# Kernel optimization log

Measured on AMD Instinct MI355X. Metric: run time of the kernel, lower is better.

The kernel has to match this reference:

```python
import jax, jax.numpy as jnp
import numpy as np

# Static configuration (mirrors TemporalAugmentation with deterministic choices)
B, T_IN, N, C = 32, 512, 543, 3
SPEED = 1.2                      # fixed draw from speed_range (0.8, 1.2)
NEW_T = int(T_IN / SPEED)        # 426
JITTER_FREQ = max(1, NEW_T // 8) # 53
FRAME_DROP_P = 0.1
JITTER_STD = 0.02
NOISE_STD = 0.01
SPATIAL_STD = 0.005


def linresample(x, out_T):
    """F.interpolate(mode='linear', align_corners=True) along last axis."""
    L = x.shape[-1]
    s = jnp.arange(out_T, dtype=x.dtype) * ((L - 1) / (out_T - 1))
    i0 = jnp.clip(jnp.floor(s).astype(jnp.int32), 0, L - 2)
    frac = s - i0.astype(x.dtype)
    return x[..., i0] * (1 - frac) + x[..., i0 + 1] * frac


def setup_inputs() -> dict:
    key = jax.random.key(0)
    k1, k2, k3, k4, k5 = jax.random.split(key, 5)
    x = jax.random.normal(k1, (B, T_IN, N, C), dtype=jnp.float32)
    mask = jnp.ones((B, T_IN), dtype=bool)
    keep_mask = jax.random.bernoulli(k2, 1.0 - FRAME_DROP_P, (B, NEW_T))
    keep_mask = keep_mask.at[:, 0].set(True).at[:, -1].set(True)
    base_jitter = jax.random.normal(k3, (B, JITTER_FREQ), dtype=jnp.float32)
    noise = jax.random.normal(k4, (B, NEW_T, N, C), dtype=jnp.float32)
    spatial_noise = jax.random.normal(k5, (B, 1, N, C), dtype=jnp.float32)
    return {"x": x, "mask": mask, "keep_mask": keep_mask,
            "base_jitter": base_jitter, "noise": noise,
            "spatial_noise": spatial_noise}


def reference(x, mask, keep_mask, base_jitter, noise, spatial_noise):
    Bb, T, Nn, Cc = x.shape
    # --- speed augment: linear resample time axis T -> NEW_T ---
    xt = jnp.moveaxis(x, 1, -1)                 # (B,N,C,T)
    x = jnp.moveaxis(linresample(xt, NEW_T), -1, 1)  # (B,NEW_T,N,C)
    # nearest resample of validity mask (PyTorch 'nearest': floor(t*in/out))
    nidx = jnp.floor(jnp.arange(NEW_T) * (T / NEW_T)).astype(jnp.int32)
    mask = mask[:, nidx]
    T2 = NEW_T
    # --- frame dropout: replace dropped frames with align_corners linear
    # resample of the kept-frame subsequence (length K) back to T2 ---
    K = keep_mask.sum(axis=1)                   # (B,) kept counts
    ar = jnp.arange(T2)
    # stable order putting kept indices first, in original order
    order = jnp.argsort(jnp.where(keep_mask, ar, T2 + ar), axis=1)  # (B,T2)
    s = ar[None, :].astype(x.dtype) * (K[:, None] - 1).astype(x.dtype) / (T2 - 1)
    r0 = jnp.clip(jnp.floor(s).astype(jnp.int32), 0, (K - 2)[:, None])
    frac = (s - r0.astype(x.dtype))[:, :, None, None]
    bidx = jnp.arange(Bb)[:, None]
    idx0 = jnp.take_along_axis(order, r0, axis=1)
    idx1 = jnp.take_along_axis(order, r0 + 1, axis=1)
    interp = x[bidx, idx0] * (1 - frac) + x[bidx, idx1] * frac
    x = jnp.where(keep_mask[:, :, None, None], x, interp)
    mask = mask & keep_mask
    # --- temporal jitter: scale per-frame velocity by smooth jitter curve ---
    jit = linresample(base_jitter * JITTER_STD, T2)   # (B,T2)
    vel = x[:, 1:] - x[:, :-1]
    x = jnp.concatenate([x[:, :1], x[:, 1:] + vel * jit[:, 1:, None, None]], axis=1)
    # --- coordinate noise + per-landmark spatial noise ---
    x = x + noise * NOISE_STD + spatial_noise * SPATIAL_STD
    return x, mask
```

## Files before the change

### kernel.cpp

```cpp
#include <hip/hip_runtime.h>
#include <stdint.h>

#define B_      32
#define T_IN_   512
#define N_      543
#define C_      3
#define NEW_T_  426
#define JF_     53
#define NC_     (N_*C_)
#define XOUT_   (B_*NEW_T_*NC_)
#define NFR_    (B_*NEW_T_)
#define GPF_    408
#define TOTG_   (NFR_*GPF_)
#define G_      4
#define NBLK_   5432

#define MODE_INT   0
#define MODE_BYTE  1
#define MODE_FLOAT 2

typedef float f4u __attribute__((vector_size(16), aligned(4)));

__device__ __forceinline__ bool read_flag(const void* p, int mode, int idx) {
    if (mode == MODE_BYTE)  return ((const uint8_t*)p)[idx] != 0;
    if (mode == MODE_FLOAT) return ((const float*)p)[idx]   != 0.0f;
    return ((const int*)p)[idx] != 0;
}

__global__ __launch_bounds__(512) void prep_kernel(
    const void* __restrict__ maskp,
    const void* __restrict__ keepp,
    const float* __restrict__ bjit,
    float* __restrict__ out_mask,
    int4*  __restrict__ wsF,
    float4* __restrict__ wsW,
    float* __restrict__ wsJ)
{
    const int b = blockIdx.x;
    const int tid = threadIdx.x;

    __shared__ int flags[6];
    __shared__ int s_mode_mask, s_mode_keep;
    if (tid < 6) flags[tid] = 0;
    __syncthreads();
    if (tid < 64) {
        uint32_t vm = ((const uint32_t*)maskp)[tid];
        uint32_t vk = ((const uint32_t*)keepp)[tid];
        if (vm == 0x3F800000u)      atomicOr(&flags[2], 1);
        else if (vm > 1u)           atomicOr(&flags[1], 1);
        if (vk == 0x3F800000u)      atomicOr(&flags[5], 1);
        else if (vk > 1u)           atomicOr(&flags[4], 1);
    }
    __syncthreads();
    if (tid == 0) {
        s_mode_mask = flags[2] ? MODE_FLOAT : (flags[1] ? MODE_BYTE : MODE_INT);
        s_mode_keep = flags[5] ? MODE_FLOAT : (flags[4] ? MODE_BYTE : MODE_INT);
    }
    __syncthreads();
    const int mmode = s_mode_mask, kmode = s_mode_keep;

    __shared__ int sk[512];
    __shared__ int ps[512];
    __shared__ int kept[NEW_T_];

    int kv = 0;
    if (tid < NEW_T_) kv = read_flag(keepp, kmode, b*NEW_T_ + tid) ? 1 : 0;
    sk[tid] = (tid < NEW_T_) ? kv : 0;
    ps[tid] = sk[tid];
    __syncthreads();
    for (int off = 1; off < 512; off <<= 1) {
        int v = (tid >= off) ? ps[tid - off] : 0;
        __syncthreads();
        ps[tid] += v;
        __syncthreads();
    }
    const int K = ps[NEW_T_ - 1];
    if (tid < NEW_T_ && kv) kept[ps[tid] - 1] = tid;
    __syncthreads();

    if (tid < NEW_T_) {
        const int t = tid;
        const float RATX = (float)(511.0 / 425.0);
        float st = (float)t * RATX;
        int i0 = (int)floorf(st);
        if (i0 < 0) i0 = 0; if (i0 > T_IN_ - 2) i0 = T_IN_ - 2;
        float w = st - (float)i0;

        int4 F; float4 W;
        if (kv) {
            F = make_int4(i0, i0 + 1, i0, i0 + 1);
            W = make_float4(1.0f - w, w, 0.0f, 0.0f);
        } else {
            float s = ((float)t * (float)(K - 1)) / 425.0f;
            int r0 = (int)floorf(s);
            if (r0 < 0) r0 = 0; if (r0 > K - 2) r0 = K - 2;
            float f = s - (float)r0;
            int j0 = kept[r0], j1 = kept[r0 + 1];
            float s0 = (float)j0 * RATX;
            int a0 = (int)floorf(s0);
            if (a0 < 0) a0 = 0; if (a0 > T_IN_ - 2) a0 = T_IN_ - 2;
            float w0 = s0 - (float)a0;
            float s1 = (float)j1 * RATX;
            int a1 = (int)floorf(s1);
            if (a1 < 0) a1 = 0; if (a1 > T_IN_ - 2) a1 = T_IN_ - 2;
            float w1 = s1 - (float)a1;
            F = make_int4(a0, a0 + 1, a1, a1 + 1);
            W = make_float4((1.0f - f) * (1.0f - w0), (1.0f - f) * w0,
                            f * (1.0f - w1),          f * w1);
        }
        const int bt = b * NEW_T_ + t;
        wsF[bt] = F;
        wsW[bt] = W;

        const float RATJ = (float)(52.0 / 425.0);
        float sj = (float)t * RATJ;
        int ji = (int)floorf(sj);
        if (ji < 0) ji = 0; if (ji > JF_ - 2) ji = JF_ - 2;
        float jf = sj - (float)ji;
        float b0 = bjit[b*JF_ + ji]     * 0.02f;
        float b1 = bjit[b*JF_ + ji + 1] * 0.02f;
        float jv = b0 * (1.0f - jf) + b1 * jf;
        if (t == 0) jv = 0.0f;
        wsJ[bt] = jv;

        float mn = (float)t * (float)(512.0 / 426.0);
        int nidx = (int)floorf(mn);
        if (nidx > T_IN_ - 1) nidx = T_IN_ - 1;
        bool mo = read_flag(maskp, mmode, b*T_IN_ + nidx) && (kv != 0);
        out_mask[bt] = mo ? 1.0f : 0.0f;
    }
}

__global__ __launch_bounds__(256) __attribute__((amdgpu_waves_per_eu(2, 8)))
void main_kernel(
    const float* __restrict__ x,
    const float* __restrict__ noise,
    const float* __restrict__ spat,
    const int4*  __restrict__ wsF,
    const float4* __restrict__ wsW,
    const float* __restrict__ wsJ,
    float* __restrict__ out)
{
    const uint32_t S = NBLK_ * 256u;
    const uint32_t g0 = blockIdx.x * 256u + threadIdx.x;

    int4   F[G_], FP[G_];
    float4 W[G_], WP[G_];
    float  JV[G_];
    uint32_t E0[G_], BT[G_], BB[G_];
    bool   VA[G_];

    #pragma unroll
    for (int k = 0; k < G_; k++) {
        uint32_t gid = g0 + (uint32_t)k * S;
        bool v = gid < (uint32_t)TOTG_;
        VA[k] = v;
        uint32_t gc = v ? gid : 0u;
        uint32_t bt = (uint32_t)(((uint64_t)gc * 673720361ull) >> 38);
        uint32_t j  = gc - bt * (uint32_t)GPF_;
        uint32_t e0 = j * 4u; if (e0 > (uint32_t)(NC_ - 4)) e0 = (uint32_t)(NC_ - 4);
        uint32_t b  = (uint32_t)(((uint64_t)bt * 161313326ull) >> 36);
        uint32_t pbt = bt ? bt - 1u : 0u;
        BT[k] = bt; BB[k] = b; E0[k] = e0;
        F[k]  = wsF[bt];  W[k]  = wsW[bt];
        FP[k] = wsF[pbt]; WP[k] = wsW[pbt];
        JV[k] = wsJ[bt];
    }

    f4u T0[G_], T1[G_], T2[G_], T3[G_], Q0[G_], Q1[G_], Q2[G_], Q3[G_], NZ[G_], SP[G_];
    #pragma unroll
    for (int k = 0; k < G_; k++) {
        const float* xb = x + (size_t)BB[k] * (T_IN_ * NC_);
        const uint32_t e0 = E0[k];
        T0[k] = *(const f4u*)(xb + (uint32_t)F[k].x  * NC_ + e0);
        T1[k] = *(const f4u*)(xb + (uint32_t)F[k].y  * NC_ + e0);
        T2[k] = *(const f4u*)(xb + (uint32_t)F[k].z  * NC_ + e0);
        T3[k] = *(const f4u*)(xb + (uint32_t)F[k].w  * NC_ + e0);
        Q0[k] = *(const f4u*)(xb + (uint32_t)FP[k].x * NC_ + e0);
        Q1[k] = *(const f4u*)(xb + (uint32_t)FP[k].y * NC_ + e0);
        Q2[k] = *(const f4u*)(xb + (uint32_t)FP[k].z * NC_ + e0);
        Q3[k] = *(const f4u*)(xb + (uint32_t)FP[k].w * NC_ + e0);
        NZ[k] = *(const f4u*)(noise + (size_t)BT[k] * NC_ + e0);
        SP[k] = *(const f4u*)(spat  + (size_t)BB[k] * NC_ + e0);
    }

    #pragma unroll
    for (int k = 0; k < G_; k++) {
        if (!VA[k]) continue;
        f4u a  = W[k].x  * T0[k] + W[k].y  * T1[k] + W[k].z  * T2[k] + W[k].w  * T3[k];
        f4u ap = WP[k].x * Q0[k] + WP[k].y * Q1[k] + WP[k].z * Q2[k] + WP[k].w * Q3[k];
        f4u r  = a + (a - ap) * JV[k] + NZ[k] * 0.01f + SP[k] * 0.005f;
        *(f4u*)(out + (size_t)BT[k] * NC_ + E0[k]) = r;
    }
}

extern "C" void kernel_launch(void* const* d_in, const int* in_sizes, int n_in,
                              void* d_out, int out_size, void* d_ws, size_t ws_size,
                              hipStream_t stream) {
    const float* x    = (const float*)d_in[0];
    const void*  mask = d_in[1];
    const void*  keep = d_in[2];
    const float* bjit = (const float*)d_in[3];
    const float* noise = (const float*)d_in[4];
    const float* spat  = (const float*)d_in[5];
    float* out = (float*)d_out;

    char* ws = (char*)d_ws;
    int4*   wsF = (int4*)ws;
    float4* wsW = (float4*)(ws + 218112);
    float*  wsJ = (float*)(ws + 436224);

    prep_kernel<<<B_, 512, 0, stream>>>(mask, keep, bjit,
                                        out + XOUT_, wsF, wsW, wsJ);
    main_kernel<<<NBLK_, 256, 0, stream>>>(x, noise, spat, wsF, wsW, wsJ, out);
}
```

Measured before the change: 269.4 us.

## Process consecutive frames per thread, reuse previous interpolation, skip zero-weight gathers

Measured after the change: 255.2 us. 5.3% less time.

```diff
diff --git a/kernel.cpp b/kernel.cpp
--- a/kernel.cpp
+++ b/kernel.cpp
@@ -11,9 +11,8 @@
 #define XOUT_   (B_*NEW_T_*NC_)
 #define NFR_    (B_*NEW_T_)
 #define GPF_    408
-#define TOTG_   (NFR_*GPF_)
-#define G_      4
-#define NBLK_   5432
+#define FPB_    6
+#define NTB_    71
 
 #define MODE_INT   0
 #define MODE_BYTE  1
@@ -131,7 +130,7 @@
     }
 }
 
-__global__ __launch_bounds__(256) __attribute__((amdgpu_waves_per_eu(2, 8)))
+__global__ __launch_bounds__(448) __attribute__((amdgpu_waves_per_eu(3, 8)))
 void main_kernel(
     const float* __restrict__ x,
     const float* __restrict__ noise,
@@ -141,56 +140,54 @@
     const float* __restrict__ wsJ,
     float* __restrict__ out)
 {
-    const uint32_t S = NBLK_ * 256u;
-    const uint32_t g0 = blockIdx.x * 256u + threadIdx.x;
-
-    int4   F[G_], FP[G_];
-    float4 W[G_], WP[G_];
-    float  JV[G_];
-    uint32_t E0[G_], BT[G_], BB[G_];
-    bool   VA[G_];
+    const int j = threadIdx.x;
+    if (j >= GPF_) return;
+    const int b  = blockIdx.y;
+    const int t0 = blockIdx.x * FPB_;
+
+    uint32_t e0 = (uint32_t)j * 4u;
+    if (e0 > (uint32_t)(NC_ - 4)) e0 = (uint32_t)(NC_ - 4);
+
+    const float* __restrict__ xb = x + (size_t)b * (T_IN_ * NC_);
+
+    const f4u sp = *(const f4u*)(spat + (size_t)b * NC_ + e0);
+
+    f4u ap;
+    {
+        const int pbt = b * NEW_T_ + (t0 ? t0 - 1 : 0);
+        const int4   Fp = wsF[pbt];
+        const float4 Wp = wsW[pbt];
+        f4u q0 = *(const f4u*)(xb + (uint32_t)Fp.x * NC_ + e0);
+        f4u q1 = *(const f4u*)(xb + (uint32_t)Fp.y * NC_ + e0);
+        ap = Wp.x * q0 + Wp.y * q1;
+        if (Wp.z != 0.0f || Wp.w != 0.0f) {
+            f4u q2 = *(const f4u*)(xb + (uint32_t)Fp.z * NC_ + e0);
+            f4u q3 = *(const f4u*)(xb + (uint32_t)Fp.w * NC_ + e0);
+            ap += Wp.z * q2 + Wp.w * q3;
+        }
+    }
 
     #pragma unroll
-    for (int k = 0; k < G_; k++) {
-        uint32_t gid = g0 + (uint32_t)k * S;
-        bool v = gid < (uint32_t)TOTG_;
-        VA[k] = v;
-        uint32_t gc = v ? gid : 0u;
-        uint32_t bt = (uint32_t)(((uint64_t)gc * 673720361ull) >> 38);
-        uint32_t j  = gc - bt * (uint32_t)GPF_;
-        uint32_t e0 = j * 4u; if (e0 > (uint32_t)(NC_ - 4)) e0 = (uint32_t)(NC_ - 4);
-        uint32_t b  = (uint32_t)(((uint64_t)bt * 161313326ull) >> 36);
-        uint32_t pbt = bt ? bt - 1u : 0u;
-        BT[k] = bt; BB[k] = b; E0[k] = e0;
-        F[k]  = wsF[bt];  W[k]  = wsW[bt];
-        FP[k] = wsF[pbt]; WP[k] = wsW[pbt];
-        JV[k] = wsJ[bt];
-    }
-
-    f4u T0[G_], T1[G_], T2[G_], T3[G_], Q0[G_], Q1[G_], Q2[G_], Q3[G_], NZ[G_], SP[G_];
-    #pragma unroll
-    for (int k = 0; k < G_; k++) {
-        const float* xb = x + (size_t)BB[k] * (T_IN_ * NC_);
-        const uint32_t e0 = E0[k];
-        T0[k] = *(const f4u*)(xb + (uint32_t)F[k].x  * NC_ + e0);
-        T1[k] = *(const f4u*)(xb + (uint32_t)F[k].y  * NC_ + e0);
-        T2[k] = *(const f4u*)(xb + (uint32_t)F[k].z  * NC_ + e0);
-        T3[k] = *(const f4u*)(xb + (uint32_t)F[k].w  * NC_ + e0);
-        Q0[k] = *(const f4u*)(xb + (uint32_t)FP[k].x * NC_ + e0);
-        Q1[k] = *(const f4u*)(xb + (uint32_t)FP[k].y * NC_ + e0);
-        Q2[k] = *(const f4u*)(xb + (uint32_t)FP[k].z * NC_ + e0);
-        Q3[k] = *(const f4u*)(xb + (uint32_t)FP[k].w * NC_ + e0);
-        NZ[k] = *(const f4u*)(noise + (size_t)BT[k] * NC_ + e0);
-        SP[k] = *(const f4u*)(spat  + (size_t)BB[k] * NC_ + e0);
-    }
-
-    #pragma unroll
-    for (int k = 0; k < G_; k++) {
-        if (!VA[k]) continue;
-        f4u a  = W[k].x  * T0[k] + W[k].y  * T1[k] + W[k].z  * T2[k] + W[k].w  * T3[k];
-        f4u ap = WP[k].x * Q0[k] + WP[k].y * Q1[k] + WP[k].z * Q2[k] + WP[k].w * Q3[k];
-        f4u r  = a + (a - ap) * JV[k] + NZ[k] * 0.01f + SP[k] * 0.005f;
-        *(f4u*)(out + (size_t)BT[k] * NC_ + E0[k]) = r;
+    for (int i = 0; i < FPB_; ++i) {
+        const int bt = b * NEW_T_ + t0 + i;
+        const int4   F = wsF[bt];
+        const float4 W = wsW[bt];
+        const float jv = wsJ[bt];
+
+        f4u nz = __builtin_nontemporal_load((const f4u*)(noise + (size_t)bt * NC_ + e0));
+
+        f4u v0 = *(const f4u*)(xb + (uint32_t)F.x * NC_ + e0);
+        f4u v1 = *(const f4u*)(xb + (uint32_t)F.y * NC_ + e0);
+        f4u a  = W.x * v0 + W.y * v1;
+        if (W.z != 0.0f || W.w != 0.0f) {
+            f4u v2 = *(const f4u*)(xb + (uint32_t)F.z * NC_ + e0);
+            f4u v3 = *(const f4u*)(xb + (uint32_t)F.w * NC_ + e0);
+            a += W.z * v2 + W.w * v3;
+        }
+
+        f4u r = a + (a - ap) * jv + nz * 0.01f + sp * 0.005f;
+        __builtin_nontemporal_store(r, (f4u*)(out + (size_t)bt * NC_ + e0));
+        ap = a;
     }
 }
 
@@ -212,5 +209,5 @@
 
     prep_kernel<<<B_, 512, 0, stream>>>(mask, keep, bjit,
                                         out + XOUT_, wsF, wsW, wsJ);
-    main_kernel<<<NBLK_, 256, 0, stream>>>(x, noise, spat, wsF, wsW, wsJ, out);
-}
+    main_kernel<<<dim3(NTB_, B_), 448, 0, stream>>>(x, noise, spat, wsF, wsW, wsJ, out);
+}
```
